# Kernel tuning notes

Hardware: AMD Instinct MI355X
Metric: run time of the kernel (lower is better)

The kernel has to match this reference:

```python
import jax, jax.numpy as jnp
import numpy as np

EPS = 1e-7  # keras backend epsilon


def setup_inputs() -> dict:
    key = jax.random.key(0)
    k1, k2, k3, k4, k5 = jax.random.split(key, 5)
    B, L, D, U = 8, 1024, 256, 256
    seq_data = jax.random.normal(k1, (B, L, D), dtype=jnp.float32)
    graph = jax.random.uniform(k2, (B, L, L), dtype=jnp.float32)
    scale = 1.0 / np.sqrt(D)
    e_weight = jax.random.normal(k3, (D, U), dtype=jnp.float32) * scale
    Wx = jax.random.normal(k4, (U, U), dtype=jnp.float32) * scale
    Wh = jax.random.normal(k5, (U, U), dtype=jnp.float32) * scale
    b = jnp.zeros((U,), dtype=jnp.float32)
    return {"seq_data": seq_data, "graph": graph, "e_weight": e_weight,
            "Wx": Wx, "Wh": Wh, "b": b}


def reference(seq_data, graph, e_weight, Wx, Wh, b):
    # beta = seq_data @ e_weight : (B, L, U)
    beta = jnp.einsum('bld,du->blu', seq_data, e_weight)
    # normalize_graph_output: divide by out-degree sum over axis 2 -> (B, L)
    norm = jnp.maximum(jnp.sum(graph, axis=2), EPS)
    beta = beta / norm[:, :, None]
    # K.batch_dot(beta(B,L,U), graph(B,L,M), axes=(1,1)) -> (B,U,M), then
    # permute (0,2,1) -> (B,M,U); fused as a single einsum.
    agg = jnp.einsum('blu,blm->bmu', beta, graph)  # (B, L, U)
    B, L, U = agg.shape
    h0 = jnp.zeros((B, U), dtype=agg.dtype)  # get_initial_state: zeros

    def step(h, x):  # SimpleRNNCell: h' = tanh(x Wx + h Wh + b)
        h = jnp.tanh(x @ Wx + h @ Wh + b)
        return h, h

    _, ys = jax.lax.scan(step, h0, jnp.swapaxes(agg, 0, 1))  # (L, B, U)
    return jnp.swapaxes(ys, 0, 1)  # (B, L, U)
```

## Files before the change

### kernel.cpp

```cpp
#include <hip/hip_runtime.h>
#include <hip/hip_bf16.h>


typedef unsigned short u16;
typedef unsigned int u32;
typedef __bf16 bf16_t;
typedef __bf16 bf16x8 __attribute__((ext_vector_type(8)));
typedef float f32x4 __attribute__((ext_vector_type(4)));
typedef unsigned short u16x8 __attribute__((ext_vector_type(8)));
typedef unsigned short u16x4 __attribute__((ext_vector_type(4)));

#define HP_B  288

struct HiLo { u16 hi, lo; };

__device__ __forceinline__ u16 f2bf(float f) {
  bf16_t h = (bf16_t)f;
  return __builtin_bit_cast(u16, h);
}
__device__ __forceinline__ HiLo splitf(float v) {
  bf16_t h = (bf16_t)v;
  HiLo r;
  r.hi = __builtin_bit_cast(u16, h);
  r.lo = f2bf(v - (float)h);
  return r;
}
__device__ __forceinline__ float tanh_fast(float x) {
  float ax = fabsf(x);
  float e  = __expf(-2.0f * ax);
  float t  = __fdividef(1.0f - e, 1.0f + e);
  return copysignf(t, x);
}
__device__ __forceinline__ void sync_lds_only() {
  __asm__ volatile("s_waitcnt lgkmcnt(0)\ns_barrier" ::: "memory");
}
__device__ __forceinline__ int swz64(int row, int col) {
  return (row << 6) + (col ^ ((((row >> 2) ^ row) & 7) << 3));
}

__global__ __launch_bounds__(512, 2) void front1(
    const float* __restrict__ Wx, u16* __restrict__ Wxth, u16* __restrict__ Wxtl,
    const float* __restrict__ Wh, u16* __restrict__ Whth, u16* __restrict__ Whtl,
    const float* __restrict__ graph, float* __restrict__ rnorm,
    const float* __restrict__ seq, const float* __restrict__ E,
    u16* __restrict__ betaTh, u16* __restrict__ betaTl) {
  __shared__ u16 Ah[64 * 64], Al[64 * 64];
  __shared__ u16 Bh[128 * 64], Bl[128 * 64];
  const int bid = blockIdx.x;
  const int t = threadIdx.x;

  if (bid >= 256 && bid < 512) {
    const int wbid = bid - 256;
    const int u = ((wbid & 127) << 1) + (t >> 8), d = t & 255;
    const float* s; u16 *dh, *dl;
    if (wbid < 128) { s = Wx; dh = Wxth; dl = Wxtl; }
    else            { s = Wh; dh = Whth; dl = Whtl; }
    HiLo r = splitf(s[d * 256 + u]);
    dh[u * 256 + d] = r.hi;
    dl[u * 256 + d] = r.lo;
    return;
  }
  if (bid >= 512) {
    const int wave = t >> 6, lane = t & 63;
    const int row = (bid - 512) * 8 + wave;
    const float* p = graph + (size_t)row * 1024 + lane * 16;
    float s = 0.f;
#pragma unroll
    for (int c = 0; c < 4; c++) {
      f32x4 v = *(const f32x4*)(p + c * 4);
#pragma unroll
      for (int j = 0; j < 4; j++) s += v[j];
    }
#pragma unroll
    for (int off = 32; off > 0; off >>= 1) s += __shfl_xor(s, off);
    if (lane == 0) rnorm[row] = 1.0f / fmaxf(s, 1e-7f);
    return;
  }

  const int v = bid;
  const int w = t >> 6, lane = t & 63, quad = lane >> 4, l16 = lane & 15;
  const int msub = w & 3, nsub = w >> 2;
  const int r0 = (v >> 1) * 64, n_base = (v & 1) * 128;
  f32x4 acc[4];
#pragma unroll
  for (int i = 0; i < 4; i++) acc[i] = (f32x4){0.f, 0.f, 0.f, 0.f};

  f32x4 rA[2], rB[4];
#pragma unroll
  for (int cc = 0; cc < 2; cc++) {
    int c = t + cc * 512;
    int r = c >> 4, c4 = c & 15;
    rA[cc] = *(const f32x4*)(seq + (size_t)(r0 + r) * 256 + c4 * 4);
  }
#pragma unroll
  for (int cc = 0; cc < 4; cc++) {
    int c = t + cc * 512;
    int r = c >> 5, c5 = c & 31;
    rB[cc] = *(const f32x4*)(E + (size_t)r * 256 + n_base + c5 * 4);
  }

  for (int kb = 0; kb < 256; kb += 64) {
#pragma unroll
    for (int cc = 0; cc < 2; cc++) {
      int c = t + cc * 512;
      int r = c >> 4, c4 = c & 15;
      u16x4 hi, lo;
#pragma unroll
      for (int j = 0; j < 4; j++) {
        HiLo s = splitf(rA[cc][j]);
        hi[j] = s.hi; lo[j] = s.lo;
      }
      *(u16x4*)(Ah + swz64(r, c4 * 4)) = hi;
      *(u16x4*)(Al + swz64(r, c4 * 4)) = lo;
    }
#pragma unroll
    for (int cc = 0; cc < 4; cc++) {
      int c = t + cc * 512;
      int r = c >> 5, c5 = c & 31;
#pragma unroll
      for (int j = 0; j < 4; j++) {
        HiLo s = splitf(rB[cc][j]);
        Bh[swz64(c5 * 4 + j, r)] = s.hi;
        Bl[swz64(c5 * 4 + j, r)] = s.lo;
      }
    }
    __syncthreads();
    if (kb + 64 < 256) {
      const int kn = kb + 64;
#pragma unroll
      for (int cc = 0; cc < 2; cc++) {
        int c = t + cc * 512;
        int r = c >> 4, c4 = c & 15;
        rA[cc] = *(const f32x4*)(seq + (size_t)(r0 + r) * 256 + kn + c4 * 4);
      }
#pragma unroll
      for (int cc = 0; cc < 4; cc++) {
        int c = t + cc * 512;
        int r = c >> 5, c5 = c & 31;
        rB[cc] = *(const f32x4*)(E + (size_t)(kn + r) * 256 + n_base + c5 * 4);
      }
    }
#pragma unroll
    for (int kk = 0; kk < 64; kk += 32) {
      bf16x8 ah = __builtin_bit_cast(bf16x8, *(const u16x8*)(Ah + swz64(msub * 16 + l16, kk + quad * 8)));
      bf16x8 al = __builtin_bit_cast(bf16x8, *(const u16x8*)(Al + swz64(msub * 16 + l16, kk + quad * 8)));
#pragma unroll
      for (int tN = 0; tN < 4; tN++) {
        int brow = nsub * 64 + tN * 16 + l16;
        bf16x8 bh = __builtin_bit_cast(bf16x8, *(const u16x8*)(Bh + swz64(brow, kk + quad * 8)));
        bf16x8 bl = __builtin_bit_cast(bf16x8, *(const u16x8*)(Bl + swz64(brow, kk + quad * 8)));
        acc[tN] = __builtin_amdgcn_mfma_f32_16x16x32_bf16(ah, bh, acc[tN], 0, 0, 0);
        acc[tN] = __builtin_amdgcn_mfma_f32_16x16x32_bf16(ah, bl, acc[tN], 0, 0, 0);
        acc[tN] = __builtin_amdgcn_mfma_f32_16x16x32_bf16(al, bh, acc[tN], 0, 0, 0);
      }
    }
    __syncthreads();
  }
  const int rbase = r0 + msub * 16 + quad * 4;
  const int bI = rbase >> 10, lI = rbase & 1023;
#pragma unroll
  for (int tN = 0; tN < 4; tN++) {
    int u = n_base + nsub * 64 + tN * 16 + l16;
    u16x4 hv, lv;
#pragma unroll
    for (int i = 0; i < 4; i++) {
      HiLo s = splitf(acc[tN][i]);
      hv[i] = s.hi; lv[i] = s.lo;
    }
    size_t off = ((size_t)bI << 18) + (size_t)u * 1024 + lI;
    *(u16x4*)(betaTh + off) = hv;
    *(u16x4*)(betaTl + off) = lv;
  }
}

__global__ __launch_bounds__(512, 2) void gemm_agg(const float* __restrict__ graph,
                                                   const u16* __restrict__ betaTh,
                                                   const u16* __restrict__ betaTl,
                                                   const float* __restrict__ rnorm,
                                                   float* __restrict__ agg) {
  __shared__ u16 Ah[64 * 64], Al[64 * 64];
  __shared__ u16 Bh[128 * 64], Bl[128 * 64];
  const int t = threadIdx.x;
  const int w = t >> 6, lane = t & 63, quad = lane >> 4, l16 = lane & 15;
  const int msub = w & 3, nsub = w >> 2;
  const int m0 = blockIdx.x * 64, n_base = blockIdx.y * 128, b = blockIdx.z;
  const float* g = graph + (size_t)b * (1024 * 1024);
  const float* rnb = rnorm + b * 1024;
  const size_t bt = (size_t)b << 18;
  f32x4 acc[4];
#pragma unroll
  for (int i = 0; i < 4; i++) acc[i] = (f32x4){0.f, 0.f, 0.f, 0.f};

  f32x4 rA[2]; float rRn[2]; u16x8 rBh[2], rBl[2];
#pragma unroll
  for (int cc = 0; cc < 2; cc++) {
    int c = t + cc * 512;
    int r = c >> 4, c4 = c & 15;
    rA[cc] = *(const f32x4*)(g + (size_t)r * 1024 + m0 + c4 * 4);
    rRn[cc] = rnb[r];
  }
#pragma unroll
  for (int cc = 0; cc < 2; cc++) {
    int c = t + cc * 512;
    int r = c >> 3, c8 = c & 7;
    rBh[cc] = *(const u16x8*)(betaTh + bt + (size_t)(n_base + r) * 1024 + c8 * 8);
    rBl[cc] = *(const u16x8*)(betaTl + bt + (size_t)(n_base + r) * 1024 + c8 * 8);
  }

  for (int kb = 0; kb < 1024; kb += 64) {
#pragma unroll
    for (int cc = 0; cc < 2; cc++) {
      int c = t + cc * 512;
      int r = c >> 4, c4 = c & 15;
#pragma unroll
      for (int j = 0; j < 4; j++) {
        HiLo s = splitf(rA[cc][j] * rRn[cc]);
        Ah[swz64(c4 * 4 + j, r)] = s.hi;
        Al[swz64(c4 * 4 + j, r)] = s.lo;
      }
    }
#pragma unroll
    for (int cc = 0; cc < 2; cc++) {
      int c = t + cc * 512;
      int r = c >> 3, c8 = c & 7;
      *(u16x8*)(Bh + swz64(r, c8 * 8)) = rBh[cc];
      *(u16x8*)(Bl + swz64(r, c8 * 8)) = rBl[cc];
    }
    __syncthreads();
    if (kb + 64 < 1024) {
      const int kn = kb + 64;
#pragma unroll
      for (int cc = 0; cc < 2; cc++) {
        int c = t + cc * 512;
        int r = c >> 4, c4 = c & 15;
        rA[cc] = *(const f32x4*)(g + (size_t)(kn + r) * 1024 + m0 + c4 * 4);
        rRn[cc] = rnb[kn + r];
      }
#pragma unroll
      for (int cc = 0; cc < 2; cc++) {
        int c = t + cc * 512;
        int r = c >> 3, c8 = c & 7;
        rBh[cc] = *(const u16x8*)(betaTh + bt + (size_t)(n_base + r) * 1024 + kn + c8 * 8);
        rBl[cc] = *(const u16x8*)(betaTl + bt + (size_t)(n_base + r) * 1024 + kn + c8 * 8);
      }
    }
#pragma unroll
    for (int kk = 0; kk < 64; kk += 32) {
      bf16x8 ah = __builtin_bit_cast(bf16x8, *(const u16x8*)(Ah + swz64(msub * 16 + l16, kk + quad * 8)));
      bf16x8 al = __builtin_bit_cast(bf16x8, *(const u16x8*)(Al + swz64(msub * 16 + l16, kk + quad * 8)));
#pragma unroll
      for (int tN = 0; tN < 4; tN++) {
        int brow = nsub * 64 + tN * 16 + l16;
        bf16x8 bh = __builtin_bit_cast(bf16x8, *(const u16x8*)(Bh + swz64(brow, kk + quad * 8)));
        bf16x8 bl = __builtin_bit_cast(bf16x8, *(const u16x8*)(Bl + swz64(brow, kk + quad * 8)));
        acc[tN] = __builtin_amdgcn_mfma_f32_16x16x32_bf16(ah, bh, acc[tN], 0, 0, 0);
        acc[tN] = __builtin_amdgcn_mfma_f32_16x16x32_bf16(ah, bl, acc[tN], 0, 0, 0);
        acc[tN] = __builtin_amdgcn_mfma_f32_16x16x32_bf16(al, bh, acc[tN], 0, 0, 0);
      }
    }
    __syncthreads();
  }
  const int mbase = m0 + msub * 16 + quad * 4;
#pragma unroll
  for (int tN = 0; tN < 4; tN++) {
    int u = n_base + nsub * 64 + tN * 16 + l16;
#pragma unroll
    for (int i = 0; i < 4; i++)
      agg[((size_t)b * 1024 + mbase + i) * 256 + u] = acc[tN][i];
  }
}

__global__ __launch_bounds__(512, 2) void gemm_xpre(const float* __restrict__ agg,
                                                    const u16* __restrict__ Wxth,
                                                    const u16* __restrict__ Wxtl,
                                                    const float* __restrict__ bias,
                                                    float* __restrict__ Xpre) {
  __shared__ u16 Ah[64 * 64], Al[64 * 64];
  __shared__ u16 Bh[128 * 64], Bl[128 * 64];
  const int t = threadIdx.x;
  const int w = t >> 6, lane = t & 63, quad = lane >> 4, l16 = lane & 15;
  const int msub = w & 3, nsub = w >> 2;
  const int r0 = blockIdx.x * 64, n_base = blockIdx.y * 128;
  f32x4 acc[4];
#pragma unroll
  for (int i = 0; i < 4; i++) acc[i] = (f32x4){0.f, 0.f, 0.f, 0.f};

  f32x4 rA[2]; u16x8 rBh[2], rBl[2];
#pragma unroll
  for (int cc = 0; cc < 2; cc++) {
    int c = t + cc * 512;
    int r = c >> 4, c4 = c & 15;
    rA[cc] = *(const f32x4*)(agg + (size_t)(r0 + r) * 256 + c4 * 4);
  }
#pragma unroll
  for (int cc = 0; cc < 2; cc++) {
    int c = t + cc * 512;
    int r = c >> 3, c8 = c & 7;
    rBh[cc] = *(const u16x8*)(Wxth + (size_t)(n_base + r) * 256 + c8 * 8);
    rBl[cc] = *(const u16x8*)(Wxtl + (size_t)(n_base + r) * 256 + c8 * 8);
  }

  for (int kb = 0; kb < 256; kb += 64) {
#pragma unroll
    for (int cc = 0; cc < 2; cc++) {
      int c = t + cc * 512;
      int r = c >> 4, c4 = c & 15;
      u16x4 hi, lo;
#pragma unroll
      for (int j = 0; j < 4; j++) {
        HiLo s = splitf(rA[cc][j]);
        hi[j] = s.hi; lo[j] = s.lo;
      }
      *(u16x4*)(Ah + swz64(r, c4 * 4)) = hi;
      *(u16x4*)(Al + swz64(r, c4 * 4)) = lo;
    }
#pragma unroll
    for (int cc = 0; cc < 2; cc++) {
      int c = t + cc * 512;
      int r = c >> 3, c8 = c & 7;
      *(u16x8*)(Bh + swz64(r, c8 * 8)) = rBh[cc];
      *(u16x8*)(Bl + swz64(r, c8 * 8)) = rBl[cc];
    }
    __syncthreads();
    if (kb + 64 < 256) {
      const int kn = kb + 64;
#pragma unroll
      for (int cc = 0; cc < 2; cc++) {
        int c = t + cc * 512;
        int r = c >> 4, c4 = c & 15;
        rA[cc] = *(const f32x4*)(agg + (size_t)(r0 + r) * 256 + kn + c4 * 4);
      }
#pragma unroll
      for (int cc = 0; cc < 2; cc++) {
        int c = t + cc * 512;
        int r = c >> 3, c8 = c & 7;
        rBh[cc] = *(const u16x8*)(Wxth + (size_t)(n_base + r) * 256 + kn + c8 * 8);
        rBl[cc] = *(const u16x8*)(Wxtl + (size_t)(n_base + r) * 256 + kn + c8 * 8);
      }
    }
#pragma unroll
    for (int kk = 0; kk < 64; kk += 32) {
      bf16x8 ah = __builtin_bit_cast(bf16x8, *(const u16x8*)(Ah + swz64(msub * 16 + l16, kk + quad * 8)));
      bf16x8 al = __builtin_bit_cast(bf16x8, *(const u16x8*)(Al + swz64(msub * 16 + l16, kk + quad * 8)));
#pragma unroll
      for (int tN = 0; tN < 4; tN++) {
        int brow = nsub * 64 + tN * 16 + l16;
        bf16x8 bh = __builtin_bit_cast(bf16x8, *(const u16x8*)(Bh + swz64(brow, kk + quad * 8)));
        bf16x8 bl = __builtin_bit_cast(bf16x8, *(const u16x8*)(Bl + swz64(brow, kk + quad * 8)));
        acc[tN] = __builtin_amdgcn_mfma_f32_16x16x32_bf16(ah, bh, acc[tN], 0, 0, 0);
        acc[tN] = __builtin_amdgcn_mfma_f32_16x16x32_bf16(ah, bl, acc[tN], 0, 0, 0);
        acc[tN] = __builtin_amdgcn_mfma_f32_16x16x32_bf16(al, bh, acc[tN], 0, 0, 0);
      }
    }
    __syncthreads();
  }
  const int rbase = r0 + msub * 16 + quad * 4;
  const int bI = rbase >> 10;
#pragma unroll
  for (int tN = 0; tN < 4; tN++) {
    int u = n_base + nsub * 64 + tN * 16 + l16;
    float bu = bias[u];
#pragma unroll
    for (int i = 0; i < 4; i++) {
      int mI = (rbase + i) & 1023;
      Xpre[((size_t)mI * 8 + bI) * 256 + u] = acc[tN][i] + bu;
    }
  }
}

__global__ __launch_bounds__(512, 2) void rnn_scan(const u16* __restrict__ Whth,
                                                   const u16* __restrict__ Whtl,
                                                   const float* __restrict__ Xpre,
                                                   float* __restrict__ out) {
  __shared__ u16 h2[2][2 * HP_B];
  const int b = blockIdx.x;
  const int t = threadIdx.x;
  const int w = t >> 6, lane = t & 63, quad = lane >> 4, l16 = lane & 15;
  const int colbase = w * 32;
  const bool epi = (quad < 2);
  const int col_e = colbase + quad * 16 + l16;

  bf16x8 bwh[2][8], bwl[2][8];
#pragma unroll
  for (int tN = 0; tN < 2; tN++) {
    const u16* wph = Whth + (size_t)(colbase + tN * 16 + l16) * 256 + quad * 8;
    const u16* wpl = Whtl + (size_t)(colbase + tN * 16 + l16) * 256 + quad * 8;
#pragma unroll
    for (int kb = 0; kb < 8; kb++) {
      bwh[tN][kb] = __builtin_bit_cast(bf16x8, *(const u16x8*)(wph + kb * 32));
      bwl[tN][kb] = __builtin_bit_cast(bf16x8, *(const u16x8*)(wpl + kb * 32));
    }
  }
  for (int i = t; i < 2 * 2 * HP_B; i += 512) ((u16*)h2)[i] = 0;

  float cb[4];
  if (epi) {
#pragma unroll
    for (int k = 0; k < 4; k++) cb[k] = Xpre[(size_t)k * 2048 + b * 256 + col_e];
  }
  const float* ldp = Xpre + 4 * 2048 + b * 256 + col_e;
  float* outp = out + (size_t)b * 262144 + col_e;
  const u16* rb0 = &h2[0][(l16 & 1) * HP_B + quad * 8];
  const u16* rb1 = &h2[1][(l16 & 1) * HP_B + quad * 8];
  u16* wb0 = &h2[0][0];
  u16* wb1 = &h2[1][0];
  __syncthreads();

  for (int m4 = 0; m4 < 1024; m4 += 4) {
#pragma unroll
    for (int k = 0; k < 4; k++) {
      const int p = k & 1;
      const u16* rb = p ? rb1 : rb0;
      u16* hw = p ? wb0 : wb1;

      bf16x8 af[8];
#pragma unroll
      for (int kb = 0; kb < 8; kb++)
        af[kb] = __builtin_bit_cast(bf16x8, *(const u16x8*)(rb + kb * 32));

      f32x4 a0a = {0.f,0.f,0.f,0.f}, a0b = {0.f,0.f,0.f,0.f};
      f32x4 a1a = {0.f,0.f,0.f,0.f}, a1b = {0.f,0.f,0.f,0.f};
#pragma unroll
      for (int kb = 0; kb < 4; kb++) {
        a0a = __builtin_amdgcn_mfma_f32_16x16x32_bf16(af[kb], bwh[0][kb], a0a, 0, 0, 0);
        a1a = __builtin_amdgcn_mfma_f32_16x16x32_bf16(af[kb], bwh[1][kb], a1a, 0, 0, 0);
        a0b = __builtin_amdgcn_mfma_f32_16x16x32_bf16(af[kb + 4], bwh[0][kb + 4], a0b, 0, 0, 0);
        a1b = __builtin_amdgcn_mfma_f32_16x16x32_bf16(af[kb + 4], bwh[1][kb + 4], a1b, 0, 0, 0);
        a0a = __builtin_amdgcn_mfma_f32_16x16x32_bf16(af[kb], bwl[0][kb], a0a, 0, 0, 0);
        a1a = __builtin_amdgcn_mfma_f32_16x16x32_bf16(af[kb], bwl[1][kb], a1a, 0, 0, 0);
        a0b = __builtin_amdgcn_mfma_f32_16x16x32_bf16(af[kb + 4], bwl[0][kb + 4], a0b, 0, 0, 0);
        a1b = __builtin_amdgcn_mfma_f32_16x16x32_bf16(af[kb + 4], bwl[1][kb + 4], a1b, 0, 0, 0);
      }

      if (epi) {
        float sA0 = quad ? a1a[0] : a0a[0];
        float sA1 = quad ? a1a[1] : a0a[1];
        float sB0 = quad ? a1b[0] : a0b[0];
        float sB1 = quad ? a1b[1] : a0b[1];
        float hi_part = sA0 + sB0;
        float lo_part = sA1 + sB1;
        float x = (hi_part + lo_part) + cb[k];
        float y = tanh_fast(x);
        HiLo s = splitf(y);
        hw[col_e] = s.hi;
        hw[HP_B + col_e] = s.lo;
        *outp = y;
        if (m4 <= 1019 - k) {
          cb[k] = *ldp;
          ldp += 2048;
        }
      }
      outp += 256;
      sync_lds_only();
    }
  }
}

extern "C" void kernel_launch(void* const* d_in, const int* in_sizes, int n_in,
                              void* d_out, int out_size, void* d_ws, size_t ws_size,
                              hipStream_t stream) {
  (void)in_sizes; (void)n_in; (void)out_size; (void)ws_size;
  const float* seq   = (const float*)d_in[0];
  const float* graph = (const float*)d_in[1];
  const float* E     = (const float*)d_in[2];
  const float* Wx    = (const float*)d_in[3];
  const float* Wh    = (const float*)d_in[4];
  const float* bias  = (const float*)d_in[5];
  float* out = (float*)d_out;

  char* w = (char*)d_ws;
  float* rnorm  = (float*)(w + 0);
  u16*   Wxth   = (u16*)(w + 294912);
  u16*   Wxtl   = (u16*)(w + 425984);
  u16*   Whth   = (u16*)(w + 557056);
  u16*   Whtl   = (u16*)(w + 688128);
  u16*   betaTh = (u16*)(w + 819200);
  u16*   betaTl = (u16*)(w + 5013504);
  float* agg    = (float*)(w + 9207808);
  float* Xpre   = (float*)(w + 17596416);

  front1<<<1536, 512, 0, stream>>>(Wx, Wxth, Wxtl, Wh, Whth, Whtl,
                                   graph, rnorm, seq, E, betaTh, betaTl);
  gemm_agg<<<dim3(16, 2, 8), 512, 0, stream>>>(graph, betaTh, betaTl, rnorm, agg);
  gemm_xpre<<<dim3(128, 2), 512, 0, stream>>>(agg, Wxth, Wxtl, bias, Xpre);
  rnn_scan<<<dim3(8), 512, 0, stream>>>(Whth, Whtl, Xpre, out);
}
```

Baseline: 747.3 us.

## Enlarge gemm_agg M tile to 128 and coarsen front1 preprocessing blocks

gemm_agg now computes a 128x128 output tile per block with each wave holding two M subtiles, halving re-reads of the beta operand but halving the grid to 128 blocks. front1's weight transpose/split and graph row-norm sections process more work per block, shrinking its grid from 1536 to 448 blocks. This trades parallelism on a 256-CU device for fewer launches and better operand reuse.

Measured after the change: 760.8 us. About the same (+1.8%).

```diff
diff --git a/kernel.cpp b/kernel.cpp
--- a/kernel.cpp
+++ b/kernel.cpp
@@ -49,31 +49,41 @@
   const int bid = blockIdx.x;
   const int t = threadIdx.x;
 
-  if (bid >= 256 && bid < 512) {
+  if (bid >= 256 && bid < 320) {
     const int wbid = bid - 256;
-    const int u = ((wbid & 127) << 1) + (t >> 8), d = t & 255;
+    const int mat = wbid >> 5;
+    const int u0 = (wbid & 31) * 8;
     const float* s; u16 *dh, *dl;
-    if (wbid < 128) { s = Wx; dh = Wxth; dl = Wxtl; }
-    else            { s = Wh; dh = Whth; dl = Whtl; }
-    HiLo r = splitf(s[d * 256 + u]);
-    dh[u * 256 + d] = r.hi;
-    dl[u * 256 + d] = r.lo;
+    if (mat == 0) { s = Wx; dh = Wxth; dl = Wxtl; }
+    else          { s = Wh; dh = Whth; dl = Whtl; }
+#pragma unroll
+    for (int jj = 0; jj < 4; jj++) {
+      int idx = t + jj * 512;
+      int u = u0 + (idx >> 8), d = idx & 255;
+      HiLo r = splitf(s[d * 256 + u]);
+      dh[u * 256 + d] = r.hi;
+      dl[u * 256 + d] = r.lo;
+    }
     return;
   }
-  if (bid >= 512) {
+  if (bid >= 320) {
     const int wave = t >> 6, lane = t & 63;
-    const int row = (bid - 512) * 8 + wave;
-    const float* p = graph + (size_t)row * 1024 + lane * 16;
-    float s = 0.f;
-#pragma unroll
-    for (int c = 0; c < 4; c++) {
-      f32x4 v = *(const f32x4*)(p + c * 4);
-#pragma unroll
-      for (int j = 0; j < 4; j++) s += v[j];
-    }
-#pragma unroll
-    for (int off = 32; off > 0; off >>= 1) s += __shfl_xor(s, off);
-    if (lane == 0) rnorm[row] = 1.0f / fmaxf(s, 1e-7f);
+    const int rbase = (bid - 320) * 64 + wave * 8;
+#pragma unroll
+    for (int rr = 0; rr < 8; rr++) {
+      const int row = rbase + rr;
+      const float* p = graph + (size_t)row * 1024 + lane * 16;
+      float s = 0.f;
+#pragma unroll
+      for (int c = 0; c < 4; c++) {
+        f32x4 v = *(const f32x4*)(p + c * 4);
+#pragma unroll
+        for (int j = 0; j < 4; j++) s += v[j];
+      }
+#pragma unroll
+      for (int off = 32; off > 0; off >>= 1) s += __shfl_xor(s, off);
+      if (lane == 0) rnorm[row] = 1.0f / fmaxf(s, 1e-7f);
+    }
     return;
   }
 
@@ -178,25 +188,27 @@
                                                    const u16* __restrict__ betaTl,
                                                    const float* __restrict__ rnorm,
                                                    float* __restrict__ agg) {
-  __shared__ u16 Ah[64 * 64], Al[64 * 64];
+  __shared__ u16 Ah[128 * 64], Al[128 * 64];
   __shared__ u16 Bh[128 * 64], Bl[128 * 64];
   const int t = threadIdx.x;
   const int w = t >> 6, lane = t & 63, quad = lane >> 4, l16 = lane & 15;
-  const int msub = w & 3, nsub = w >> 2;
-  const int m0 = blockIdx.x * 64, n_base = blockIdx.y * 128, b = blockIdx.z;
+  const int msub4 = w & 3, nsub2 = w >> 2;
+  const int m0 = blockIdx.x * 128, n_base = blockIdx.y * 128, b = blockIdx.z;
   const float* g = graph + (size_t)b * (1024 * 1024);
   const float* rnb = rnorm + b * 1024;
   const size_t bt = (size_t)b << 18;
-  f32x4 acc[4];
-#pragma unroll
-  for (int i = 0; i < 4; i++) acc[i] = (f32x4){0.f, 0.f, 0.f, 0.f};
-
-  f32x4 rA[2]; float rRn[2]; u16x8 rBh[2], rBl[2];
-#pragma unroll
-  for (int cc = 0; cc < 2; cc++) {
+  f32x4 acc[2][4];
+#pragma unroll
+  for (int mt = 0; mt < 2; mt++)
+#pragma unroll
+    for (int i = 0; i < 4; i++) acc[mt][i] = (f32x4){0.f, 0.f, 0.f, 0.f};
+
+  f32x4 rA[4]; float rRn[4]; u16x8 rBh[2], rBl[2];
+#pragma unroll
+  for (int cc = 0; cc < 4; cc++) {
     int c = t + cc * 512;
-    int r = c >> 4, c4 = c & 15;
-    rA[cc] = *(const f32x4*)(g + (size_t)r * 1024 + m0 + c4 * 4);
+    int r = c >> 5, c5 = c & 31;
+    rA[cc] = *(const f32x4*)(g + (size_t)r * 1024 + m0 + c5 * 4);
     rRn[cc] = rnb[r];
   }
 #pragma unroll
@@ -209,14 +221,14 @@
 
   for (int kb = 0; kb < 1024; kb += 64) {
 #pragma unroll
-    for (int cc = 0; cc < 2; cc++) {
+    for (int cc = 0; cc < 4; cc++) {
       int c = t + cc * 512;
-      int r = c >> 4, c4 = c & 15;
+      int r = c >> 5, c5 = c & 31;
 #pragma unroll
       for (int j = 0; j < 4; j++) {
         HiLo s = splitf(rA[cc][j] * rRn[cc]);
-        Ah[swz64(c4 * 4 + j, r)] = s.hi;
-        Al[swz64(c4 * 4 + j, r)] = s.lo;
+        Ah[swz64(c5 * 4 + j, r)] = s.hi;
+        Al[swz64(c5 * 4 + j, r)] = s.lo;
       }
     }
 #pragma unroll
@@ -230,10 +242,10 @@
     if (kb + 64 < 1024) {
       const int kn = kb + 64;
 #pragma unroll
-      for (int cc = 0; cc < 2; cc++) {
+      for (int cc = 0; cc < 4; cc++) {
         int c = t + cc * 512;
-        int r = c >> 4, c4 = c & 15;
-        rA[cc] = *(const f32x4*)(g + (size_t)(kn + r) * 1024 + m0 + c4 * 4);
+        int r = c >> 5, c5 = c & 31;
+        rA[cc] = *(const f32x4*)(g + (size_t)(kn + r) * 1024 + m0 + c5 * 4);
         rRn[cc] = rnb[kn + r];
       }
 #pragma unroll
@@ -246,27 +258,34 @@
     }
 #pragma unroll
     for (int kk = 0; kk < 64; kk += 32) {
-      bf16x8 ah = __builtin_bit_cast(bf16x8, *(const u16x8*)(Ah + swz64(msub * 16 + l16, kk + quad * 8)));
-      bf16x8 al = __builtin_bit_cast(bf16x8, *(const u16x8*)(Al + swz64(msub * 16 + l16, kk + quad * 8)));
-#pragma unroll
-      for (int tN = 0; tN < 4; tN++) {
-        int brow = nsub * 64 + tN * 16 + l16;
-        bf16x8 bh = __builtin_bit_cast(bf16x8, *(const u16x8*)(Bh + swz64(brow, kk + quad * 8)));
-        bf16x8 bl = __builtin_bit_cast(bf16x8, *(const u16x8*)(Bl + swz64(brow, kk + quad * 8)));
-        acc[tN] = __builtin_amdgcn_mfma_f32_16x16x32_bf16(ah, bh, acc[tN], 0, 0, 0);
-        acc[tN] = __builtin_amdgcn_mfma_f32_16x16x32_bf16(ah, bl, acc[tN], 0, 0, 0);
-        acc[tN] = __builtin_amdgcn_mfma_f32_16x16x32_bf16(al, bh, acc[tN], 0, 0, 0);
+#pragma unroll
+      for (int mt = 0; mt < 2; mt++) {
+        int arow = msub4 * 32 + mt * 16 + l16;
+        bf16x8 ah = __builtin_bit_cast(bf16x8, *(const u16x8*)(Ah + swz64(arow, kk + quad * 8)));
+        bf16x8 al = __builtin_bit_cast(bf16x8, *(const u16x8*)(Al + swz64(arow, kk + quad * 8)));
+#pragma unroll
+        for (int tN = 0; tN < 4; tN++) {
+          int brow = nsub2 * 64 + tN * 16 + l16;
+          bf16x8 bh = __builtin_bit_cast(bf16x8, *(const u16x8*)(Bh + swz64(brow, kk + quad * 8)));
+          bf16x8 bl = __builtin_bit_cast(bf16x8, *(const u16x8*)(Bl + swz64(brow, kk + quad * 8)));
+          acc[mt][tN] = __builtin_amdgcn_mfma_f32_16x16x32_bf16(ah, bh, acc[mt][tN], 0, 0, 0);
+          acc[mt][tN] = __builtin_amdgcn_mfma_f32_16x16x32_bf16(ah, bl, acc[mt][tN], 0, 0, 0);
+          acc[mt][tN] = __builtin_amdgcn_mfma_f32_16x16x32_bf16(al, bh, acc[mt][tN], 0, 0, 0);
+        }
       }
     }
     __syncthreads();
   }
-  const int mbase = m0 + msub * 16 + quad * 4;
-#pragma unroll
-  for (int tN = 0; tN < 4; tN++) {
-    int u = n_base + nsub * 64 + tN * 16 + l16;
-#pragma unroll
-    for (int i = 0; i < 4; i++)
-      agg[((size_t)b * 1024 + mbase + i) * 256 + u] = acc[tN][i];
+#pragma unroll
+  for (int mt = 0; mt < 2; mt++) {
+    const int mbase = m0 + msub4 * 32 + mt * 16 + quad * 4;
+#pragma unroll
+    for (int tN = 0; tN < 4; tN++) {
+      int u = n_base + nsub2 * 64 + tN * 16 + l16;
+#pragma unroll
+      for (int i = 0; i < 4; i++)
+        agg[((size_t)b * 1024 + mbase + i) * 256 + u] = acc[mt][tN][i];
+    }
   }
 }
 
@@ -479,9 +498,9 @@
   float* agg    = (float*)(w + 9207808);
   float* Xpre   = (float*)(w + 17596416);
 
-  front1<<<1536, 512, 0, stream>>>(Wx, Wxth, Wxtl, Wh, Whth, Whtl,
-                                   graph, rnorm, seq, E, betaTh, betaTl);
-  gemm_agg<<<dim3(16, 2, 8), 512, 0, stream>>>(graph, betaTh, betaTl, rnorm, agg);
+  front1<<<448, 512, 0, stream>>>(Wx, Wxth, Wxtl, Wh, Whth, Whtl,
+                                  graph, rnorm, seq, E, betaTh, betaTl);
+  gemm_agg<<<dim3(8, 2, 8), 512, 0, stream>>>(graph, betaTh, betaTl, rnorm, agg);
   gemm_xpre<<<dim3(128, 2), 512, 0, stream>>>(agg, Wxth, Wxtl, bias, Xpre);
   rnn_scan<<<dim3(8), 512, 0, stream>>>(Whth, Whtl, Xpre, out);
 }
```
